# Kernel optimization log

Measured on AMD Instinct MI355X. Metric: run time of the kernel, lower is better.

Reference implementation:

```python
import jax, jax.numpy as jnp
import numpy as np

NUM_GRAPHS = 1000


def gcn_conv(x, src, dst, n_nodes, W, b):
    """PyG GCNConv: symmetric normalization with self-loops, then scatter-add."""
    # self-loops already appended to src/dst by caller
    deg = jax.ops.segment_sum(jnp.ones_like(dst, dtype=x.dtype), dst, num_segments=n_nodes)
    dinv = jnp.where(deg > 0, jax.lax.rsqrt(deg), 0.0)
    norm = dinv[src] * dinv[dst]                      # [E+N]
    h = x @ W.T                                       # [N, out]
    msg = h[src] * norm[:, None]                      # gather + scale
    out = jax.ops.segment_sum(msg, dst, num_segments=n_nodes)
    return out + b


def setup_inputs() -> dict:
    key = jax.random.key(0)
    ks = jax.random.split(key, 9)
    N, E = 100000, 1600000
    x = jax.random.normal(ks[0], (N, 32), dtype=jnp.float32)
    edge_index = jax.random.randint(ks[1], (2, E), 0, N, dtype=jnp.int64)
    batch = jnp.sort(jax.random.randint(ks[2], (N,), 0, NUM_GRAPHS, dtype=jnp.int64))
    # parameters (Glorot-ish scale)
    W1 = jax.random.normal(ks[3], (16, 32), dtype=jnp.float32) * (1.0 / np.sqrt(32))
    b1 = jnp.zeros((16,), dtype=jnp.float32)
    W2 = jax.random.normal(ks[4], (16, 16), dtype=jnp.float32) * (1.0 / np.sqrt(16))
    b2 = jnp.zeros((16,), dtype=jnp.float32)
    Wl = jax.random.normal(ks[5], (5, 16), dtype=jnp.float32) * (1.0 / np.sqrt(16))
    bl = jnp.zeros((5,), dtype=jnp.float32)
    return {"x": x, "edge_index": edge_index, "batch": batch,
            "W1": W1, "b1": b1, "W2": W2, "b2": b2, "Wl": Wl, "bl": bl}


def reference(x, edge_index, batch, W1, b1, W2, b2, Wl, bl):
    n_nodes = x.shape[0]
    loops = jnp.arange(n_nodes, dtype=edge_index.dtype)
    src = jnp.concatenate([edge_index[0], loops])
    dst = jnp.concatenate([edge_index[1], loops])

    h = gcn_conv(x, src, dst, n_nodes, W1, b1)
    h = jax.nn.relu(h)
    h = gcn_conv(h, src, dst, n_nodes, W2, b2)

    # global mean pool over graphs
    sums = jax.ops.segment_sum(h, batch, num_segments=NUM_GRAPHS)
    cnts = jax.ops.segment_sum(jnp.ones((n_nodes,), dtype=h.dtype), batch, num_segments=NUM_GRAPHS)
    pooled = sums / jnp.maximum(cnts, 1.0)[:, None]   # [G, 16]

    logits = pooled @ Wl.T + bl                       # [G, 5]
    return jax.nn.softmax(logits, axis=-1)
```

## Files before the change

kernel.cpp:

```cpp
#include <hip/hip_runtime.h>
#include <hip/hip_fp16.h>
#include <math.h>

#define NG 1000
#define NPN 512
#define PSH 9
#define MAXPART 256
#define K1BLK 256

__global__ void zero_kernel(int4* __restrict__ p, int n4) {
    int i = blockIdx.x * blockDim.x + threadIdx.x;
    if (i < n4) p[i] = make_int4(0, 0, 0, 0);
}

__global__ void __launch_bounds__(256) pcount_kernel(const int* __restrict__ dst,
                                                     int* __restrict__ pcnt,
                                                     int E, int CH, int NPART) {
    __shared__ int h[MAXPART];
    int b = blockIdx.x, t = threadIdx.x;
    h[t] = 0;
    __syncthreads();
    int beg = b * CH, end = min(E, beg + CH);
    for (int e = beg + t; e < end; e += 256) atomicAdd(&h[dst[e] >> PSH], 1);
    __syncthreads();
    if (t < NPART && h[t] > 0) atomicAdd(&pcnt[t], h[t]);
}

__global__ void __launch_bounds__(256) pscan_kernel(const int* __restrict__ pcnt,
                                                    int* __restrict__ poff,
                                                    int* __restrict__ pcur,
                                                    int* __restrict__ rowptr,
                                                    int NPART, int N, int E) {
    __shared__ int sm[256];
    int t = threadIdx.x;
    int v = (t < NPART) ? pcnt[t] : 0;
    sm[t] = v;
    __syncthreads();
    for (int o = 1; o < 256; o <<= 1) {
        int u = (t >= o) ? sm[t - o] : 0;
        __syncthreads();
        sm[t] += u;
        __syncthreads();
    }
    int ex = sm[t] - v;
    if (t < NPART) { poff[t] = ex; pcur[t] = ex; }
    if (t == NPART - 1) poff[NPART] = ex + v;
    if (t == 0) rowptr[N] = E;
}

__global__ void __launch_bounds__(256) pscatter_kernel(const int* __restrict__ src,
                                                       const int* __restrict__ dst,
                                                       int* __restrict__ pcur,
                                                       int* __restrict__ ibuf,
                                                       int E, int CH, int NPART) {
    __shared__ int h[MAXPART];
    __shared__ int gbase[MAXPART];
    int b = blockIdx.x, t = threadIdx.x;
    h[t] = 0;
    __syncthreads();
    int beg = b * CH, end = min(E, beg + CH);
    for (int e = beg + t; e < end; e += 256) atomicAdd(&h[dst[e] >> PSH], 1);
    __syncthreads();
    if (t < NPART) gbase[t] = (h[t] > 0) ? atomicAdd(&pcur[t], h[t]) : 0;
    __syncthreads();
    h[t] = 0;
    __syncthreads();
    for (int e = beg + t; e < end; e += 256) {
        int s = src[e], d = dst[e];
        int p = d >> PSH;
        int pos = gbase[p] + atomicAdd(&h[p], 1);
        ibuf[pos] = ((d & (NPN - 1)) << 17) | s;
    }
}

__global__ void __launch_bounds__(256) part_kernel(const int* __restrict__ poff,
                                                   const int* __restrict__ ibuf,
                                                   int* __restrict__ csr,
                                                   int* __restrict__ rowptr,
                                                   float* __restrict__ dinv, int N) {
    __shared__ int h[NPN];
    __shared__ int ex[NPN];
    __shared__ int cur[NPN];
    __shared__ int sm[256];
    int p = blockIdx.x, t = threadIdx.x;
    int base = p * NPN;
    for (int k = t; k < NPN; k += 256) h[k] = 0;
    __syncthreads();
    int ebeg = poff[p], eend = poff[p + 1];
    for (int e = ebeg + t; e < eend; e += 256) atomicAdd(&h[ibuf[e] >> 17], 1);
    __syncthreads();
    int a0 = h[2 * t], a1 = h[2 * t + 1];
    int s = a0 + a1;
    sm[t] = s;
    __syncthreads();
    for (int o = 1; o < 256; o <<= 1) {
        int u = (t >= o) ? sm[t - o] : 0;
        __syncthreads();
        sm[t] += u;
        __syncthreads();
    }
    int exc = sm[t] - s;
    ex[2 * t] = exc;          cur[2 * t] = exc;
    ex[2 * t + 1] = exc + a0; cur[2 * t + 1] = exc + a0;
    __syncthreads();
    for (int k = t; k < NPN; k += 256) {
        int n = base + k;
        if (n < N) {
            rowptr[n] = ebeg + ex[k];
            dinv[n] = rsqrtf((float)h[k] + 1.0f);
        }
    }
    for (int e = ebeg + t; e < eend; e += 256) {
        int w = ibuf[e];
        int ln = w >> 17;
        int pos = ebeg + atomicAdd(&cur[ln], 1);
        csr[pos] = w & 0x1FFFF;
    }
}

__global__ void xform1_kernel(const float* __restrict__ X, const float* __restrict__ W,
                              const float* __restrict__ dinv, __half* __restrict__ A1h, int N) {
    __shared__ float sW[16 * 32];
    for (int t = threadIdx.x; t < 512; t += blockDim.x) sW[t] = W[t];
    __syncthreads();
    int i = blockIdx.x * blockDim.x + threadIdx.x;
    if (i >= N) return;
    float xv[32];
    const float4* xp = (const float4*)(X + (size_t)i * 32);
#pragma unroll
    for (int q = 0; q < 8; q++) {
        float4 v = xp[q];
        xv[4*q+0] = v.x; xv[4*q+1] = v.y; xv[4*q+2] = v.z; xv[4*q+3] = v.w;
    }
    float dd = dinv[i];
    union { __half2 h2[8]; uint4 u4[2]; } pk;
#pragma unroll
    for (int j2 = 0; j2 < 8; j2++) {
        float o[2];
#pragma unroll
        for (int jj = 0; jj < 2; jj++) {
            int j = j2 * 2 + jj;
            float a = 0.f;
#pragma unroll
            for (int k = 0; k < 32; k++) a += xv[k] * sW[j * 32 + k];
            o[jj] = a * dd;
        }
        pk.h2[j2] = __floats2half2_rn(o[0], o[1]);
    }
    uint4* yp = (uint4*)(A1h + (size_t)i * 16);
    yp[0] = pk.u4[0];
    yp[1] = pk.u4[1];
}

__device__ __forceinline__ float4 h2f4(uint2 v) {
    float2 f0 = __half22float2(*(const __half2*)&v.x);
    float2 f1 = __half22float2(*(const __half2*)&v.y);
    return make_float4(f0.x, f0.y, f1.x, f1.y);
}

__global__ void __launch_bounds__(256) agg1_kernel(
    const int* __restrict__ rowptr, const int* __restrict__ csr,
    const float* __restrict__ dinv, const __half* __restrict__ A1h,
    const float* __restrict__ b1, const float* __restrict__ W2,
    __half* __restrict__ A2h, int N) {
    __shared__ float sW2[256];
    __shared__ float sb1[16];
    __shared__ float tile[64][17];
    int t = threadIdx.x;
    int team = t >> 2, q = t & 3;
    int node = blockIdx.x * 64 + team;
    sW2[t] = W2[t];
    if (t < 16) sb1[t] = b1[t];
    __syncthreads();
    const uint2* H2 = (const uint2*)A1h;
    float4 acc = make_float4(0.f, 0.f, 0.f, 0.f);
    float dd = 0.f;
    if (node < N) {
        dd = dinv[node];
        float4 sv = h2f4(H2[(size_t)node * 4 + q]);
        acc = sv;
        int e = rowptr[node], end = rowptr[node + 1];
        for (; e + 1 < end; e += 2) {
            int s0 = csr[e], s1 = csr[e + 1];
            float4 g0 = h2f4(H2[(size_t)s0 * 4 + q]);
            float4 g1 = h2f4(H2[(size_t)s1 * 4 + q]);
            acc.x += g0.x + g1.x; acc.y += g0.y + g1.y;
            acc.z += g0.z + g1.z; acc.w += g0.w + g1.w;
        }
        if (e < end) {
            float4 g = h2f4(H2[(size_t)csr[e] * 4 + q]);
            acc.x += g.x; acc.y += g.y; acc.z += g.z; acc.w += g.w;
        }
        tile[team][q*4+0] = fmaxf(acc.x * dd + sb1[q*4+0], 0.f);
        tile[team][q*4+1] = fmaxf(acc.y * dd + sb1[q*4+1], 0.f);
        tile[team][q*4+2] = fmaxf(acc.z * dd + sb1[q*4+2], 0.f);
        tile[team][q*4+3] = fmaxf(acc.w * dd + sb1[q*4+3], 0.f);
    }
    __syncthreads();
    if (node < N) {
        float o[4];
#pragma unroll
        for (int jj = 0; jj < 4; jj++) {
            int j = q * 4 + jj;
            float a = 0.f;
#pragma unroll
            for (int k = 0; k < 16; k++) a += tile[team][k] * sW2[j * 16 + k];
            o[jj] = a * dd;
        }
        uint2 ov;
        *(__half2*)&ov.x = __floats2half2_rn(o[0], o[1]);
        *(__half2*)&ov.y = __floats2half2_rn(o[2], o[3]);
        ((uint2*)A2h)[(size_t)node * 4 + q] = ov;
    }
}

__global__ void __launch_bounds__(256) agg2_kernel(
    const int* __restrict__ rowptr, const int* __restrict__ csr,
    const float* __restrict__ dinv, const __half* __restrict__ A2h,
    const int* __restrict__ batch, float* __restrict__ pooled,
    float* __restrict__ cnt, int N) {
    __shared__ float tile[64][17];
    __shared__ int gb[64];
    int t = threadIdx.x;
    int team = t >> 2, q = t & 3;
    int base = blockIdx.x * 64;
    int node = base + team;
    if (t < 64) {
        int n = base + t;
        gb[t] = (n < N) ? batch[n] : -1;
    }
    const uint2* H2 = (const uint2*)A2h;
    if (node < N) {
        float dd = dinv[node];
        float4 acc = h2f4(H2[(size_t)node * 4 + q]);
        int e = rowptr[node], end = rowptr[node + 1];
        for (; e + 1 < end; e += 2) {
            int s0 = csr[e], s1 = csr[e + 1];
            float4 g0 = h2f4(H2[(size_t)s0 * 4 + q]);
            float4 g1 = h2f4(H2[(size_t)s1 * 4 + q]);
            acc.x += g0.x + g1.x; acc.y += g0.y + g1.y;
            acc.z += g0.z + g1.z; acc.w += g0.w + g1.w;
        }
        if (e < end) {
            float4 g = h2f4(H2[(size_t)csr[e] * 4 + q]);
            acc.x += g.x; acc.y += g.y; acc.z += g.z; acc.w += g.w;
        }
        tile[team][q*4+0] = acc.x * dd;
        tile[team][q*4+1] = acc.y * dd;
        tile[team][q*4+2] = acc.z * dd;
        tile[team][q*4+3] = acc.w * dd;
    }
    __syncthreads();
    int nmax = N - base; if (nmax > 64) nmax = 64;
    if (t < 16 && nmax > 0) {
        int c = t;
        int g = gb[0];
        float a = 0.f, k = 0.f;
        for (int n = 0; n < nmax; n++) {
            int gi = gb[n];
            if (gi != g) {
                atomicAdd(&pooled[(size_t)g * 16 + c], a);
                if (c == 0) atomicAdd(&cnt[g], k);
                a = 0.f; k = 0.f; g = gi;
            }
            a += tile[n][c];
            k += 1.f;
        }
        atomicAdd(&pooled[(size_t)g * 16 + c], a);
        if (c == 0) atomicAdd(&cnt[g], k);
    }
}

__global__ void head_kernel(const float* __restrict__ pooled, const float* __restrict__ cnt,
                            const float* __restrict__ b2, const float* __restrict__ Wl,
                            const float* __restrict__ bl, float* __restrict__ out) {
    int g = blockIdx.x * blockDim.x + threadIdx.x;
    if (g >= NG) return;
    float c = cnt[g];
    c = c > 1.0f ? c : 1.0f;
    float inv = 1.0f / c;
    float p[16];
#pragma unroll
    for (int j = 0; j < 16; j++) p[j] = pooled[(size_t)g * 16 + j] * inv + b2[j];
    float logits[5], m = -INFINITY;
#pragma unroll
    for (int r = 0; r < 5; r++) {
        float a = bl[r];
#pragma unroll
        for (int j = 0; j < 16; j++) a += p[j] * Wl[r * 16 + j];
        logits[r] = a;
        m = fmaxf(m, a);
    }
    float s = 0.f;
#pragma unroll
    for (int r = 0; r < 5; r++) { logits[r] = expf(logits[r] - m); s += logits[r]; }
    float is = 1.0f / s;
#pragma unroll
    for (int r = 0; r < 5; r++) out[(size_t)g * 5 + r] = logits[r] * is;
}

static inline size_t rnd16b(size_t bytes) { return (bytes + 15) & ~(size_t)15; }

extern "C" void kernel_launch(void* const* d_in, const int* in_sizes, int n_in,
                              void* d_out, int out_size, void* d_ws, size_t ws_size,
                              hipStream_t stream) {
    const float* x     = (const float*)d_in[0];
    const int*   edge  = (const int*)d_in[1];
    const int*   batch = (const int*)d_in[2];
    const float* W1    = (const float*)d_in[3];
    const float* b1    = (const float*)d_in[4];
    const float* W2    = (const float*)d_in[5];
    const float* b2    = (const float*)d_in[6];
    const float* Wl    = (const float*)d_in[7];
    const float* bl    = (const float*)d_in[8];

    const int N = in_sizes[0] / 32;
    const int E = in_sizes[1] / 2;
    const int* src = edge;
    const int* dst = edge + E;

    const int NPART = (N + NPN - 1) / NPN;
    const int CH = (E + K1BLK - 1) / K1BLK;

    char* ws = (char*)d_ws;
    size_t off = 0;
    int*      pcnt   = (int*)(ws + off);      off += rnd16b((size_t)MAXPART * 4);
    float*    pooled = (float*)(ws + off);    off += rnd16b((size_t)NG * 16 * 4);
    float*    cnt    = (float*)(ws + off);    off += rnd16b((size_t)NG * 4);
    size_t zbytes = off;
    int*      poff   = (int*)(ws + off);      off += rnd16b((size_t)(MAXPART + 1) * 4);
    int*      pcur   = (int*)(ws + off);      off += rnd16b((size_t)MAXPART * 4);
    int*      rowptr = (int*)(ws + off);      off += rnd16b((size_t)(N + 1) * 4);
    float*    dinv   = (float*)(ws + off);    off += rnd16b((size_t)N * 4);
    int*      ibuf   = (int*)(ws + off);      off += rnd16b((size_t)E * 4);
    int*      csr    = (int*)(ws + off);      off += rnd16b((size_t)E * 4);
    __half*   A1h    = (__half*)(ws + off);   off += rnd16b((size_t)N * 16 * 2);
    __half*   A2h    = (__half*)(ws + off);   off += rnd16b((size_t)N * 16 * 2);

    int n4 = (int)(zbytes / 16);
    zero_kernel<<<(n4 + 255) / 256, 256, 0, stream>>>((int4*)d_ws, n4);

    const int BS = 256;
    int gN = (N + BS - 1) / BS;

    pcount_kernel<<<K1BLK, 256, 0, stream>>>(dst, pcnt, E, CH, NPART);
    pscan_kernel<<<1, 256, 0, stream>>>(pcnt, poff, pcur, rowptr, NPART, N, E);
    pscatter_kernel<<<K1BLK, 256, 0, stream>>>(src, dst, pcur, ibuf, E, CH, NPART);
    part_kernel<<<NPART, 256, 0, stream>>>(poff, ibuf, csr, rowptr, dinv, N);

    xform1_kernel<<<gN, BS, 0, stream>>>(x, W1, dinv, A1h, N);
    int gAgg = (N + 63) / 64;
    agg1_kernel<<<gAgg, 256, 0, stream>>>(rowptr, csr, dinv, A1h, b1, W2, A2h, N);
    agg2_kernel<<<gAgg, 256, 0, stream>>>(rowptr, csr, dinv, A2h, batch, pooled, cnt, N);
    head_kernel<<<(NG + BS - 1) / BS, BS, 0, stream>>>(pooled, cnt, b2, Wl, bl, (float*)d_out);
}
```

Before: 120.5 us.

## Fuse layer-1 transform into partition kernel and widen aggregation gathers to 16B

The first-layer feature transform (X·W1ᵀ scaled by dinv, stored as fp16) moves into the tail of part_kernel, where each block already holds the per-node degree counts. This removes one kernel launch and a dinv reload. The two aggregation kernels now use 2 threads per node with 16-byte uint4 gathers and a 4-way unrolled edge loop, instead of 4 threads with 8-byte loads, so each block covers 128 nodes. The cost is that only 196 partition blocks do the transform, which reduces its parallelism, and the aggregation threads use more registers.

```diff
diff --git a/kernel.cpp b/kernel.cpp
--- a/kernel.cpp
+++ b/kernel.cpp
@@ -77,14 +77,20 @@
                                                    const int* __restrict__ ibuf,
                                                    int* __restrict__ csr,
                                                    int* __restrict__ rowptr,
-                                                   float* __restrict__ dinv, int N) {
+                                                   float* __restrict__ dinv,
+                                                   const float* __restrict__ X,
+                                                   const float* __restrict__ W1,
+                                                   __half* __restrict__ A1h, int N) {
     __shared__ int h[NPN];
     __shared__ int ex[NPN];
     __shared__ int cur[NPN];
     __shared__ int sm[256];
+    __shared__ float sW1[512];
     int p = blockIdx.x, t = threadIdx.x;
     int base = p * NPN;
     for (int k = t; k < NPN; k += 256) h[k] = 0;
+    sW1[t] = W1[t];
+    sW1[t + 256] = W1[t + 256];
     __syncthreads();
     int ebeg = poff[p], eend = poff[p + 1];
     for (int e = ebeg + t; e < eend; e += 256) atomicAdd(&h[ibuf[e] >> 17], 1);
@@ -116,46 +122,43 @@
         int pos = ebeg + atomicAdd(&cur[ln], 1);
         csr[pos] = w & 0x1FFFF;
     }
-}
-
-__global__ void xform1_kernel(const float* __restrict__ X, const float* __restrict__ W,
-                              const float* __restrict__ dinv, __half* __restrict__ A1h, int N) {
-    __shared__ float sW[16 * 32];
-    for (int t = threadIdx.x; t < 512; t += blockDim.x) sW[t] = W[t];
-    __syncthreads();
-    int i = blockIdx.x * blockDim.x + threadIdx.x;
-    if (i >= N) return;
-    float xv[32];
-    const float4* xp = (const float4*)(X + (size_t)i * 32);
-#pragma unroll
-    for (int q = 0; q < 8; q++) {
-        float4 v = xp[q];
-        xv[4*q+0] = v.x; xv[4*q+1] = v.y; xv[4*q+2] = v.z; xv[4*q+3] = v.w;
-    }
-    float dd = dinv[i];
-    union { __half2 h2[8]; uint4 u4[2]; } pk;
-#pragma unroll
-    for (int j2 = 0; j2 < 8; j2++) {
-        float o[2];
-#pragma unroll
-        for (int jj = 0; jj < 2; jj++) {
-            int j = j2 * 2 + jj;
-            float a = 0.f;
-#pragma unroll
-            for (int k = 0; k < 32; k++) a += xv[k] * sW[j * 32 + k];
-            o[jj] = a * dd;
-        }
-        pk.h2[j2] = __floats2half2_rn(o[0], o[1]);
-    }
-    uint4* yp = (uint4*)(A1h + (size_t)i * 16);
-    yp[0] = pk.u4[0];
-    yp[1] = pk.u4[1];
-}
-
-__device__ __forceinline__ float4 h2f4(uint2 v) {
-    float2 f0 = __half22float2(*(const __half2*)&v.x);
-    float2 f1 = __half22float2(*(const __half2*)&v.y);
-    return make_float4(f0.x, f0.y, f1.x, f1.y);
+    for (int k = t; k < NPN; k += 256) {
+        int n = base + k;
+        if (n >= N) continue;
+        float dd = rsqrtf((float)h[k] + 1.0f);
+        float xv[32];
+        const float4* xp = (const float4*)(X + (size_t)n * 32);
+#pragma unroll
+        for (int qq = 0; qq < 8; qq++) {
+            float4 v = xp[qq];
+            xv[4*qq+0] = v.x; xv[4*qq+1] = v.y; xv[4*qq+2] = v.z; xv[4*qq+3] = v.w;
+        }
+        union { __half2 h2[8]; uint4 u4[2]; } pk;
+#pragma unroll
+        for (int j2 = 0; j2 < 8; j2++) {
+            float o[2];
+#pragma unroll
+            for (int jj = 0; jj < 2; jj++) {
+                int j = j2 * 2 + jj;
+                float a = 0.f;
+#pragma unroll
+                for (int kk = 0; kk < 32; kk++) a += xv[kk] * sW1[j * 32 + kk];
+                o[jj] = a * dd;
+            }
+            pk.h2[j2] = __floats2half2_rn(o[0], o[1]);
+        }
+        uint4* yp = (uint4*)(A1h + (size_t)n * 16);
+        yp[0] = pk.u4[0];
+        yp[1] = pk.u4[1];
+    }
+}
+
+__device__ __forceinline__ void add8(float* a, uint4 v) {
+    float2 f;
+    f = __half22float2(*(const __half2*)&v.x); a[0] += f.x; a[1] += f.y;
+    f = __half22float2(*(const __half2*)&v.y); a[2] += f.x; a[3] += f.y;
+    f = __half22float2(*(const __half2*)&v.z); a[4] += f.x; a[5] += f.y;
+    f = __half22float2(*(const __half2*)&v.w); a[6] += f.x; a[7] += f.y;
 }
 
 __global__ void __launch_bounds__(256) agg1_kernel(
@@ -165,52 +168,50 @@
     __half* __restrict__ A2h, int N) {
     __shared__ float sW2[256];
     __shared__ float sb1[16];
-    __shared__ float tile[64][17];
+    __shared__ float tile[128][17];
     int t = threadIdx.x;
-    int team = t >> 2, q = t & 3;
-    int node = blockIdx.x * 64 + team;
+    int team = t >> 1, q = t & 1;
+    int node = blockIdx.x * 128 + team;
     sW2[t] = W2[t];
     if (t < 16) sb1[t] = b1[t];
     __syncthreads();
-    const uint2* H2 = (const uint2*)A1h;
-    float4 acc = make_float4(0.f, 0.f, 0.f, 0.f);
+    const uint4* H4 = (const uint4*)A1h;
     float dd = 0.f;
     if (node < N) {
         dd = dinv[node];
-        float4 sv = h2f4(H2[(size_t)node * 4 + q]);
-        acc = sv;
+        float acc[8] = {0.f,0.f,0.f,0.f,0.f,0.f,0.f,0.f};
+        add8(acc, H4[(size_t)node * 2 + q]);
         int e = rowptr[node], end = rowptr[node + 1];
-        for (; e + 1 < end; e += 2) {
-            int s0 = csr[e], s1 = csr[e + 1];
-            float4 g0 = h2f4(H2[(size_t)s0 * 4 + q]);
-            float4 g1 = h2f4(H2[(size_t)s1 * 4 + q]);
-            acc.x += g0.x + g1.x; acc.y += g0.y + g1.y;
-            acc.z += g0.z + g1.z; acc.w += g0.w + g1.w;
-        }
-        if (e < end) {
-            float4 g = h2f4(H2[(size_t)csr[e] * 4 + q]);
-            acc.x += g.x; acc.y += g.y; acc.z += g.z; acc.w += g.w;
-        }
-        tile[team][q*4+0] = fmaxf(acc.x * dd + sb1[q*4+0], 0.f);
-        tile[team][q*4+1] = fmaxf(acc.y * dd + sb1[q*4+1], 0.f);
-        tile[team][q*4+2] = fmaxf(acc.z * dd + sb1[q*4+2], 0.f);
-        tile[team][q*4+3] = fmaxf(acc.w * dd + sb1[q*4+3], 0.f);
+        for (; e + 3 < end; e += 4) {
+            int s0 = csr[e], s1 = csr[e+1], s2 = csr[e+2], s3 = csr[e+3];
+            uint4 g0 = H4[(size_t)s0 * 2 + q];
+            uint4 g1 = H4[(size_t)s1 * 2 + q];
+            uint4 g2 = H4[(size_t)s2 * 2 + q];
+            uint4 g3 = H4[(size_t)s3 * 2 + q];
+            add8(acc, g0); add8(acc, g1); add8(acc, g2); add8(acc, g3);
+        }
+        for (; e < end; e++) add8(acc, H4[(size_t)csr[e] * 2 + q]);
+#pragma unroll
+        for (int j = 0; j < 8; j++)
+            tile[team][q * 8 + j] = fmaxf(acc[j] * dd + sb1[q * 8 + j], 0.f);
     }
     __syncthreads();
     if (node < N) {
-        float o[4];
-#pragma unroll
-        for (int jj = 0; jj < 4; jj++) {
-            int j = q * 4 + jj;
+        float o[8];
+#pragma unroll
+        for (int jj = 0; jj < 8; jj++) {
+            int j = q * 8 + jj;
             float a = 0.f;
 #pragma unroll
             for (int k = 0; k < 16; k++) a += tile[team][k] * sW2[j * 16 + k];
             o[jj] = a * dd;
         }
-        uint2 ov;
-        *(__half2*)&ov.x = __floats2half2_rn(o[0], o[1]);
-        *(__half2*)&ov.y = __floats2half2_rn(o[2], o[3]);
-        ((uint2*)A2h)[(size_t)node * 4 + q] = ov;
+        uint4 ov;
+        ((__half2*)&ov)[0] = __floats2half2_rn(o[0], o[1]);
+        ((__half2*)&ov)[1] = __floats2half2_rn(o[2], o[3]);
+        ((__half2*)&ov)[2] = __floats2half2_rn(o[4], o[5]);
+        ((__half2*)&ov)[3] = __floats2half2_rn(o[6], o[7]);
+        ((uint4*)A2h)[(size_t)node * 2 + q] = ov;
     }
 }
 
@@ -219,39 +220,36 @@
     const float* __restrict__ dinv, const __half* __restrict__ A2h,
     const int* __restrict__ batch, float* __restrict__ pooled,
     float* __restrict__ cnt, int N) {
-    __shared__ float tile[64][17];
-    __shared__ int gb[64];
+    __shared__ float tile[128][17];
+    __shared__ int gb[128];
     int t = threadIdx.x;
-    int team = t >> 2, q = t & 3;
-    int base = blockIdx.x * 64;
+    int team = t >> 1, q = t & 1;
+    int base = blockIdx.x * 128;
     int node = base + team;
-    if (t < 64) {
+    if (t < 128) {
         int n = base + t;
         gb[t] = (n < N) ? batch[n] : -1;
     }
-    const uint2* H2 = (const uint2*)A2h;
+    const uint4* H4 = (const uint4*)A2h;
     if (node < N) {
         float dd = dinv[node];
-        float4 acc = h2f4(H2[(size_t)node * 4 + q]);
+        float acc[8] = {0.f,0.f,0.f,0.f,0.f,0.f,0.f,0.f};
+        add8(acc, H4[(size_t)node * 2 + q]);
         int e = rowptr[node], end = rowptr[node + 1];
-        for (; e + 1 < end; e += 2) {
-            int s0 = csr[e], s1 = csr[e + 1];
-            float4 g0 = h2f4(H2[(size_t)s0 * 4 + q]);
-            float4 g1 = h2f4(H2[(size_t)s1 * 4 + q]);
-            acc.x += g0.x + g1.x; acc.y += g0.y + g1.y;
-            acc.z += g0.z + g1.z; acc.w += g0.w + g1.w;
-        }
-        if (e < end) {
-            float4 g = h2f4(H2[(size_t)csr[e] * 4 + q]);
-            acc.x += g.x; acc.y += g.y; acc.z += g.z; acc.w += g.w;
-        }
-        tile[team][q*4+0] = acc.x * dd;
-        tile[team][q*4+1] = acc.y * dd;
-        tile[team][q*4+2] = acc.z * dd;
-        tile[team][q*4+3] = acc.w * dd;
-    }
-    __syncthreads();
-    int nmax = N - base; if (nmax > 64) nmax = 64;
+        for (; e + 3 < end; e += 4) {
+            int s0 = csr[e], s1 = csr[e+1], s2 = csr[e+2], s3 = csr[e+3];
+            uint4 g0 = H4[(size_t)s0 * 2 + q];
+            uint4 g1 = H4[(size_t)s1 * 2 + q];
+            uint4 g2 = H4[(size_t)s2 * 2 + q];
+            uint4 g3 = H4[(size_t)s3 * 2 + q];
+            add8(acc, g0); add8(acc, g1); add8(acc, g2); add8(acc, g3);
+        }
+        for (; e < end; e++) add8(acc, H4[(size_t)csr[e] * 2 + q]);
+#pragma unroll
+        for (int j = 0; j < 8; j++) tile[team][q * 8 + j] = acc[j] * dd;
+    }
+    __syncthreads();
+    int nmax = N - base; if (nmax > 128) nmax = 128;
     if (t < 16 && nmax > 0) {
         int c = t;
         int g = gb[0];
@@ -340,17 +338,13 @@
     int n4 = (int)(zbytes / 16);
     zero_kernel<<<(n4 + 255) / 256, 256, 0, stream>>>((int4*)d_ws, n4);
 
-    const int BS = 256;
-    int gN = (N + BS - 1) / BS;
-
     pcount_kernel<<<K1BLK, 256, 0, stream>>>(dst, pcnt, E, CH, NPART);
     pscan_kernel<<<1, 256, 0, stream>>>(pcnt, poff, pcur, rowptr, NPART, N, E);
     pscatter_kernel<<<K1BLK, 256, 0, stream>>>(src, dst, pcur, ibuf, E, CH, NPART);
-    part_kernel<<<NPART, 256, 0, stream>>>(poff, ibuf, csr, rowptr, dinv, N);
-
-    xform1_kernel<<<gN, BS, 0, stream>>>(x, W1, dinv, A1h, N);
-    int gAgg = (N + 63) / 64;
+    part_kernel<<<NPART, 256, 0, stream>>>(poff, ibuf, csr, rowptr, dinv, x, W1, A1h, N);
+
+    int gAgg = (N + 127) / 128;
     agg1_kernel<<<gAgg, 256, 0, stream>>>(rowptr, csr, dinv, A1h, b1, W2, A2h, N);
     agg2_kernel<<<gAgg, 256, 0, stream>>>(rowptr, csr, dinv, A2h, batch, pooled, cnt, N);
-    head_kernel<<<(NG + BS - 1) / BS, BS, 0, stream>>>(pooled, cnt, b2, Wl, bl, (float*)d_out);
-}
+    head_kernel<<<(NG + 255) / 256, 256, 0, stream>>>(pooled, cnt, b2, Wl, bl, (float*)d_out);
+}
```

New measurement: 118.4 us. About the same (-1.7%).
